# Kernel optimization log

Hardware: AMD Instinct MI355X
Metric: run time of the kernel (lower is better)

Reference implementation:

```python
import jax, jax.numpy as jnp
import numpy as np

B, Q, K, H = 4, 256, 256, 512
NEG = -1e9


def setup_inputs() -> dict:
    key = jax.random.key(0)
    ks = jax.random.split(key, 7)
    scale = 1.0 / np.sqrt(H)
    return {
        "query": jax.random.normal(ks[0], (B, Q, H), jnp.float32),
        "key": jax.random.normal(ks[1], (B, K, H), jnp.float32),
        "value": jax.random.normal(ks[2], (B, K, H), jnp.float32),
        "valid_lens": jax.random.randint(ks[3], (B,), 0, K, jnp.int32),
        "Wq": jax.random.normal(ks[4], (H, H), jnp.float32) * scale,
        "Wk": jax.random.normal(ks[5], (H, H), jnp.float32) * scale,
        "wv": jax.random.normal(ks[6], (H,), jnp.float32) * scale,
    }


def reference(query, key, value, valid_lens, Wq, Wk, wv):
    # projections (nn.Linear without bias)
    q = query @ Wq              # [B,Q,H]
    k = key @ Wk                # [B,K,H]
    # broadcast add + tanh: [B,Q,K,H]
    features = jnp.tanh(q[:, :, None, :] + k[:, None, :, :])
    # score projection w_v: [B,Q,K]
    scores = jnp.einsum("bqkh,h->bqk", features, wv)
    # sequence mask: positions >= valid_len masked out
    mask = jnp.arange(K)[None, :] >= valid_lens[:, None]   # [B,K]
    scores = jnp.where(mask[:, None, :], NEG, scores)
    attn = jax.nn.softmax(scores, axis=-1)                 # [B,Q,K]
    context = jnp.einsum("bqk,bkh->bqh", attn, value)      # [B,Q,H]
    return context
```

## Files before the change

kernel.cpp:

```cpp
#include <hip/hip_runtime.h>
#include <hip/hip_bf16.h>

#define B_ 4
#define Q_ 256
#define K_ 256
#define H_ 512
#define NEG (-1e9f)
#define PRESCALE 2.885390081777927f

typedef _Float16 half8 __attribute__((ext_vector_type(8)));
typedef float    f32x4 __attribute__((ext_vector_type(4)));

__global__ __launch_bounds__(256) void proj_kernel(
    const float* __restrict__ Xq, const float* __restrict__ Xk,
    const float* __restrict__ Wq, const float* __restrict__ Wk,
    float* __restrict__ Eq, float* __restrict__ EkT,
    const int* __restrict__ vlen)
{
    const int bx   = blockIdx.x;
    const int z    = bx >> 4;
    const int row0 = (bx & 15) * 64;
    const int bb   = row0 >> 8;
    const int k0   = row0 & 255;
    if (z && k0 >= vlen[bb]) return;

    const float* X = z ? Xk : Xq;
    const float* W = z ? Wk : Wq;

    __shared__ _Float16 Xl[4 * 520];
    __shared__ _Float16 Wl[4 * 520];

    const int col0 = blockIdx.y * 64;
    const int t    = threadIdx.x;
    const int lane = t & 63;
    const int w    = t >> 6;
    const int m    = lane & 15;
    const int kgl  = lane >> 4;

    const int xr  = t >> 2;
    const int xkg = t & 3;
    const int wc  = t & 63;
    const int wkg = t >> 6;

    f32x4 acc[4] = {};

    float4 xv0 = *(const float4*)&X[(size_t)(row0 + xr) * H_ + xkg * 8];
    float4 xv1 = *(const float4*)&X[(size_t)(row0 + xr) * H_ + xkg * 8 + 4];
    float wv8[8];
    #pragma unroll
    for (int i = 0; i < 8; ++i)
        wv8[i] = W[(size_t)(wkg * 8 + i) * H_ + col0 + wc];

    for (int it = 0; it < 16; ++it) {
        {
            half8 hx;
            hx[0] = (_Float16)xv0.x; hx[1] = (_Float16)xv0.y;
            hx[2] = (_Float16)xv0.z; hx[3] = (_Float16)xv0.w;
            hx[4] = (_Float16)xv1.x; hx[5] = (_Float16)xv1.y;
            hx[6] = (_Float16)xv1.z; hx[7] = (_Float16)xv1.w;
            *(half8*)&Xl[xkg * 520 + xr * 8] = hx;
            half8 hw;
            #pragma unroll
            for (int i = 0; i < 8; ++i) hw[i] = (_Float16)wv8[i];
            *(half8*)&Wl[wkg * 520 + wc * 8] = hw;
        }
        __syncthreads();
        if (it < 15) {
            const int kk = (it + 1) * 32;
            xv0 = *(const float4*)&X[(size_t)(row0 + xr) * H_ + kk + xkg * 8];
            xv1 = *(const float4*)&X[(size_t)(row0 + xr) * H_ + kk + xkg * 8 + 4];
            #pragma unroll
            for (int i = 0; i < 8; ++i)
                wv8[i] = W[(size_t)(kk + wkg * 8 + i) * H_ + col0 + wc];
        }
        const _Float16* Asrc = z ? Wl : Xl;
        const _Float16* Bsrc = z ? Xl : Wl;
        const half8 af = *(const half8*)&Asrc[kgl * 520 + (16 * w + m) * 8];
        #pragma unroll
        for (int nt = 0; nt < 4; ++nt) {
            const half8 bf = *(const half8*)&Bsrc[kgl * 520 + (nt * 16 + m) * 8];
            acc[nt] = __builtin_amdgcn_mfma_f32_16x16x32_f16(af, bf, acc[nt], 0, 0, 0);
        }
        __syncthreads();
    }

    if (!z) {
        #pragma unroll
        for (int nt = 0; nt < 4; ++nt) {
            const int gcol = col0 + nt * 16 + m;
            #pragma unroll
            for (int r = 0; r < 4; ++r) {
                const int grow = row0 + 16 * w + kgl * 4 + r;
                Eq[(size_t)grow * H_ + gcol] =
                    __builtin_amdgcn_exp2f(acc[nt][r] * PRESCALE);
            }
        }
    } else {
        #pragma unroll
        for (int nt = 0; nt < 4; ++nt) {
            const int gk = k0 + nt * 16 + m;
            #pragma unroll
            for (int r = 0; r < 4; ++r) {
                const int gh = col0 + 16 * w + kgl * 4 + r;
                EkT[((size_t)bb * H_ + gh) * K_ + gk] =
                    __builtin_amdgcn_exp2f(acc[nt][r] * PRESCALE);
            }
        }
    }
}

__global__ __launch_bounds__(512) void fused_attn(
    const float* __restrict__ Eq, const float* __restrict__ EkT,
    const float* __restrict__ value, const int* __restrict__ vlen,
    const float* __restrict__ wv, float* __restrict__ out)
{
    const int qt = blockIdx.x;
    const int b  = blockIdx.y;
    const int q0 = qt * 2;
    const int t    = threadIdx.x;
    const int wave = t >> 6;
    const int lane = t & 63;

    __shared__ float eqh[H_][2];
    __shared__ float wm[H_];
    __shared__ float sc[2][K_];
    __shared__ float ctxp[4][2][H_];

    const int valid = vlen[b];

    if (t < 256) {
        const int qi = t >> 7, p4 = (t & 127) * 4;
        const float4 v = *(const float4*)&Eq[((size_t)b * Q_ + q0 + qi) * H_ + p4];
        eqh[p4 + 0][qi] = v.x; eqh[p4 + 1][qi] = v.y;
        eqh[p4 + 2][qi] = v.z; eqh[p4 + 3][qi] = v.w;
    } else if (t < 384) {
        const int i = (t - 256) * 4;
        const float4 w = *(const float4*)&wv[i];
        *(float4*)&wm[i] = make_float4(-2.f * w.x, -2.f * w.y, -2.f * w.z, -2.f * w.w);
    }
    __syncthreads();

    const int band = wave * 32;
    const int ho   = lane >> 3;
    const int kg   = lane & 7;
    const int kq   = band + kg * 4;

    if (band < valid) {
        const float* ekp = EkT + ((size_t)b * H_ + ho) * K_ + kq;
        float a0[4] = {}, a1[4] = {};
        float4 pe[4], ne[4];
        #pragma unroll
        for (int p = 0; p < 4; ++p)
            pe[p] = *(const float4*)(ekp + (size_t)p * 8 * K_);

        for (int g = 0; g < 16; ++g) {
            if (g < 15) {
                #pragma unroll
                for (int p = 0; p < 4; ++p)
                    ne[p] = *(const float4*)(ekp + (size_t)((g + 1) * 4 + p) * 8 * K_);
            }
            #pragma unroll
            for (int p = 0; p < 4; ++p) {
                const int h = ho + 8 * (g * 4 + p);
                const float2 eq = *(const float2*)&eqh[h][0];
                const float  w  = wm[h];
                const float ek4[4] = {pe[p].x, pe[p].y, pe[p].z, pe[p].w};
                #pragma unroll
                for (int j = 0; j < 4; ++j) {
                    const float g0 = __builtin_fmaf(eq.x, ek4[j], 1.0f);
                    a0[j] = __builtin_fmaf(w, __builtin_amdgcn_rcpf(g0), a0[j]);
                    const float g1 = __builtin_fmaf(eq.y, ek4[j], 1.0f);
                    a1[j] = __builtin_fmaf(w, __builtin_amdgcn_rcpf(g1), a1[j]);
                }
            }
            if (g < 15) {
                #pragma unroll
                for (int p = 0; p < 4; ++p) pe[p] = ne[p];
            }
        }
        #pragma unroll
        for (int d = 8; d < 64; d <<= 1) {
            #pragma unroll
            for (int j = 0; j < 4; ++j) {
                a0[j] += __shfl_xor(a0[j], d);
                a1[j] += __shfl_xor(a1[j], d);
            }
        }
        if (ho == 0) {
            *(float4*)&sc[0][kq] = make_float4(a0[0], a0[1], a0[2], a0[3]);
            *(float4*)&sc[1][kq] = make_float4(a1[0], a1[1], a1[2], a1[3]);
        }
    }
    __syncthreads();

    if (wave < 2) {
        const int q = wave;
        if (valid == 0) {
            #pragma unroll
            for (int j = 0; j < 4; ++j) sc[q][lane + 64 * j] = 1.0f / K_;
        } else {
            float sv[4], mx = -3e38f;
            #pragma unroll
            for (int j = 0; j < 4; ++j) {
                const int kk = lane + 64 * j;
                const float s = (kk < valid) ? sc[q][kk] : NEG;
                sv[j] = s;
                mx = fmaxf(mx, s);
            }
            #pragma unroll
            for (int d = 32; d; d >>= 1) mx = fmaxf(mx, __shfl_xor(mx, d));
            float ev[4], sum = 0.f;
            #pragma unroll
            for (int j = 0; j < 4; ++j) { ev[j] = __expf(sv[j] - mx); sum += ev[j]; }
            #pragma unroll
            for (int d = 32; d; d >>= 1) sum += __shfl_xor(sum, d);
            const float inv = 1.0f / sum;
            #pragma unroll
            for (int j = 0; j < 4; ++j) sc[q][lane + 64 * j] = ev[j] * inv;
        }
    }
    __syncthreads();

    const int klim = (valid == 0) ? K_ : valid;
    const int kb   = wave * 32;
    const int kend = min(32, klim - kb);
    const int h0   = lane * 8;

    float c0[8] = {}, c1[8] = {};
    for (int kc = 0; kc < kend; ++kc) {
        const int kk = kb + kc;
        const float4* vp = (const float4*)&value[((size_t)b * K_ + kk) * H_ + h0];
        const float4 v0 = vp[0], v1 = vp[1];
        const float vr[8] = {v0.x, v0.y, v0.z, v0.w, v1.x, v1.y, v1.z, v1.w};
        const float a0 = sc[0][kk], a1 = sc[1][kk];
        #pragma unroll
        for (int j = 0; j < 8; ++j) {
            c0[j] = __builtin_fmaf(a0, vr[j], c0[j]);
            c1[j] = __builtin_fmaf(a1, vr[j], c1[j]);
        }
    }

    #define PARK(s)                                                         \
        do {                                                                \
            float* d0 = &ctxp[s][0][h0];                                    \
            float* d1 = &ctxp[s][1][h0];                                    \
            ((float4*)d0)[0] = make_float4(c0[0], c0[1], c0[2], c0[3]);     \
            ((float4*)d0)[1] = make_float4(c0[4], c0[5], c0[6], c0[7]);     \
            ((float4*)d1)[0] = make_float4(c1[0], c1[1], c1[2], c1[3]);     \
            ((float4*)d1)[1] = make_float4(c1[4], c1[5], c1[6], c1[7]);     \
        } while (0)
    #define FOLD(s)                                                         \
        do {                                                                \
            const float* d0 = &ctxp[s][0][h0];                              \
            const float* d1 = &ctxp[s][1][h0];                              \
            _Pragma("unroll")                                               \
            for (int j = 0; j < 8; ++j) { c0[j] += d0[j]; c1[j] += d1[j]; } \
        } while (0)

    if (wave >= 4) PARK(wave - 4);
    __syncthreads();
    if (wave < 4) FOLD(wave);
    __syncthreads();
    if (wave == 2 || wave == 3) PARK(wave - 2);
    __syncthreads();
    if (wave < 2) FOLD(wave);
    __syncthreads();
    if (wave == 1) PARK(1);
    __syncthreads();
    if (wave == 0) {
        FOLD(1);
        float* o0 = &out[((size_t)b * Q_ + q0 + 0) * H_ + h0];
        float* o1 = &out[((size_t)b * Q_ + q0 + 1) * H_ + h0];
        ((float4*)o0)[0] = make_float4(c0[0], c0[1], c0[2], c0[3]);
        ((float4*)o0)[1] = make_float4(c0[4], c0[5], c0[6], c0[7]);
        ((float4*)o1)[0] = make_float4(c1[0], c1[1], c1[2], c1[3]);
        ((float4*)o1)[1] = make_float4(c1[4], c1[5], c1[6], c1[7]);
    }
    #undef PARK
    #undef FOLD
}

extern "C" void kernel_launch(void* const* d_in, const int* in_sizes, int n_in,
                              void* d_out, int out_size, void* d_ws, size_t ws_size,
                              hipStream_t stream)
{
    const float* query = (const float*)d_in[0];
    const float* key   = (const float*)d_in[1];
    const float* value = (const float*)d_in[2];
    const int*   vlen  = (const int*)  d_in[3];
    const float* Wq    = (const float*)d_in[4];
    const float* Wk    = (const float*)d_in[5];
    const float* wv    = (const float*)d_in[6];
    float*       outp  = (float*)d_out;

    float* EqBuf  = (float*)d_ws;
    float* EkTBuf = EqBuf + (size_t)B_ * Q_ * H_;

    dim3 g1(32, 8);
    proj_kernel<<<g1, 256, 0, stream>>>(query, key, Wq, Wk, EqBuf, EkTBuf, vlen);

    dim3 g2(Q_ / 2, B_);
    fused_attn<<<g2, 512, 0, stream>>>(EqBuf, EkTBuf, value, vlen, wv, outp);
}
```

Measured before the change: 40.18 us.

## Double-buffer projection GEMM with 512 threads, deepen EkT prefetch, relayout LDS

The projection kernel now runs 512 threads with a 2x4 wave tiling, K-step 64, and double-buffered LDS, which removes the trailing barrier per iteration and halves loop trips. In the attention kernel, the Eq and weight vectors are relaid out in LDS so each thread reads contiguous float4s per group instead of scattered float2/float loads. The EkT prefetch is also deepened to two groups ahead. The cost is more registers and larger LDS, which could lower occupancy.

```diff
diff --git a/kernel.cpp b/kernel.cpp
--- a/kernel.cpp
+++ b/kernel.cpp
@@ -11,7 +11,7 @@
 typedef _Float16 half8 __attribute__((ext_vector_type(8)));
 typedef float    f32x4 __attribute__((ext_vector_type(4)));
 
-__global__ __launch_bounds__(256) void proj_kernel(
+__global__ __launch_bounds__(512) void proj_kernel(
     const float* __restrict__ Xq, const float* __restrict__ Xk,
     const float* __restrict__ Wq, const float* __restrict__ Wk,
     float* __restrict__ Eq, float* __restrict__ EkT,
@@ -27,84 +27,88 @@
     const float* X = z ? Xk : Xq;
     const float* W = z ? Wk : Wq;
 
-    __shared__ _Float16 Xl[4 * 520];
-    __shared__ _Float16 Wl[4 * 520];
+    __shared__ _Float16 Xl[2][8 * 520];
+    __shared__ _Float16 Wl[2][8 * 520];
 
     const int col0 = blockIdx.y * 64;
     const int t    = threadIdx.x;
     const int lane = t & 63;
-    const int w    = t >> 6;
+    const int wave = t >> 6;
+    const int mw   = wave >> 1;
+    const int nw   = wave & 1;
     const int m    = lane & 15;
     const int kgl  = lane >> 4;
 
-    const int xr  = t >> 2;
-    const int xkg = t & 3;
-    const int wc  = t & 63;
-    const int wkg = t >> 6;
-
-    f32x4 acc[4] = {};
-
-    float4 xv0 = *(const float4*)&X[(size_t)(row0 + xr) * H_ + xkg * 8];
-    float4 xv1 = *(const float4*)&X[(size_t)(row0 + xr) * H_ + xkg * 8 + 4];
+    const int xr = t >> 3;
+    const int xg = t & 7;
+    const int wc = t & 63;
+    const int wg = t >> 6;
+
+    f32x4 acc[2] = {};
+
+    float4 xv0 = *(const float4*)&X[(size_t)(row0 + xr) * H_ + xg * 8];
+    float4 xv1 = *(const float4*)&X[(size_t)(row0 + xr) * H_ + xg * 8 + 4];
     float wv8[8];
     #pragma unroll
     for (int i = 0; i < 8; ++i)
-        wv8[i] = W[(size_t)(wkg * 8 + i) * H_ + col0 + wc];
-
-    for (int it = 0; it < 16; ++it) {
+        wv8[i] = W[(size_t)(wg * 8 + i) * H_ + col0 + wc];
+
+    for (int it = 0; it < 8; ++it) {
+        const int buf = it & 1;
         {
             half8 hx;
             hx[0] = (_Float16)xv0.x; hx[1] = (_Float16)xv0.y;
             hx[2] = (_Float16)xv0.z; hx[3] = (_Float16)xv0.w;
             hx[4] = (_Float16)xv1.x; hx[5] = (_Float16)xv1.y;
             hx[6] = (_Float16)xv1.z; hx[7] = (_Float16)xv1.w;
-            *(half8*)&Xl[xkg * 520 + xr * 8] = hx;
+            *(half8*)&Xl[buf][xg * 520 + xr * 8] = hx;
             half8 hw;
             #pragma unroll
             for (int i = 0; i < 8; ++i) hw[i] = (_Float16)wv8[i];
-            *(half8*)&Wl[wkg * 520 + wc * 8] = hw;
+            *(half8*)&Wl[buf][wg * 520 + wc * 8] = hw;
         }
         __syncthreads();
-        if (it < 15) {
-            const int kk = (it + 1) * 32;
-            xv0 = *(const float4*)&X[(size_t)(row0 + xr) * H_ + kk + xkg * 8];
-            xv1 = *(const float4*)&X[(size_t)(row0 + xr) * H_ + kk + xkg * 8 + 4];
+        if (it < 7) {
+            const int kk = (it + 1) * 64;
+            xv0 = *(const float4*)&X[(size_t)(row0 + xr) * H_ + kk + xg * 8];
+            xv1 = *(const float4*)&X[(size_t)(row0 + xr) * H_ + kk + xg * 8 + 4];
             #pragma unroll
             for (int i = 0; i < 8; ++i)
-                wv8[i] = W[(size_t)(kk + wkg * 8 + i) * H_ + col0 + wc];
-        }
-        const _Float16* Asrc = z ? Wl : Xl;
-        const _Float16* Bsrc = z ? Xl : Wl;
-        const half8 af = *(const half8*)&Asrc[kgl * 520 + (16 * w + m) * 8];
-        #pragma unroll
-        for (int nt = 0; nt < 4; ++nt) {
-            const half8 bf = *(const half8*)&Bsrc[kgl * 520 + (nt * 16 + m) * 8];
-            acc[nt] = __builtin_amdgcn_mfma_f32_16x16x32_f16(af, bf, acc[nt], 0, 0, 0);
-        }
-        __syncthreads();
-    }
-
+                wv8[i] = W[(size_t)(kk + wg * 8 + i) * H_ + col0 + wc];
+        }
+        const _Float16* Asrc = z ? &Wl[buf][0] : &Xl[buf][0];
+        const _Float16* Bsrc = z ? &Xl[buf][0] : &Wl[buf][0];
+        #pragma unroll
+        for (int ks = 0; ks < 2; ++ks) {
+            const int slab = (ks * 4 + kgl) * 520;
+            const half8 af = *(const half8*)&Asrc[slab + (16 * mw + m) * 8];
+            #pragma unroll
+            for (int nt = 0; nt < 2; ++nt) {
+                const half8 bf =
+                    *(const half8*)&Bsrc[slab + (nw * 32 + nt * 16 + m) * 8];
+                acc[nt] = __builtin_amdgcn_mfma_f32_16x16x32_f16(af, bf, acc[nt], 0, 0, 0);
+            }
+        }
+    }
+
+    const int rloc = 16 * mw + kgl * 4;
     if (!z) {
         #pragma unroll
-        for (int nt = 0; nt < 4; ++nt) {
-            const int gcol = col0 + nt * 16 + m;
-            #pragma unroll
-            for (int r = 0; r < 4; ++r) {
-                const int grow = row0 + 16 * w + kgl * 4 + r;
-                Eq[(size_t)grow * H_ + gcol] =
+        for (int nt = 0; nt < 2; ++nt) {
+            const int gcol = col0 + nw * 32 + nt * 16 + m;
+            #pragma unroll
+            for (int r = 0; r < 4; ++r)
+                Eq[(size_t)(row0 + rloc + r) * H_ + gcol] =
                     __builtin_amdgcn_exp2f(acc[nt][r] * PRESCALE);
-            }
         }
     } else {
         #pragma unroll
-        for (int nt = 0; nt < 4; ++nt) {
-            const int gk = k0 + nt * 16 + m;
-            #pragma unroll
-            for (int r = 0; r < 4; ++r) {
-                const int gh = col0 + 16 * w + kgl * 4 + r;
-                EkT[((size_t)bb * H_ + gh) * K_ + gk] =
+        for (int nt = 0; nt < 2; ++nt) {
+            const int gk = k0 + nw * 32 + nt * 16 + m;
+            #pragma unroll
+            for (int r = 0; r < 4; ++r)
+                EkT[((size_t)bb * H_ + col0 + rloc + r) * K_ + gk] =
                     __builtin_amdgcn_exp2f(acc[nt][r] * PRESCALE);
-            }
         }
     }
 }
@@ -121,8 +125,8 @@
     const int wave = t >> 6;
     const int lane = t & 63;
 
-    __shared__ float eqh[H_][2];
-    __shared__ float wm[H_];
+    __shared__ float eqh2[8 * 132];
+    __shared__ float wm2[8 * 68];
     __shared__ float sc[2][K_];
     __shared__ float ctxp[4][2][H_];
 
@@ -131,12 +135,21 @@
     if (t < 256) {
         const int qi = t >> 7, p4 = (t & 127) * 4;
         const float4 v = *(const float4*)&Eq[((size_t)b * Q_ + q0 + qi) * H_ + p4];
-        eqh[p4 + 0][qi] = v.x; eqh[p4 + 1][qi] = v.y;
-        eqh[p4 + 2][qi] = v.z; eqh[p4 + 3][qi] = v.w;
+        const float vv[4] = {v.x, v.y, v.z, v.w};
+        #pragma unroll
+        for (int j = 0; j < 4; ++j) {
+            const int h = p4 + j;
+            eqh2[(h & 7) * 132 + (h >> 3) * 2 + qi] = vv[j];
+        }
     } else if (t < 384) {
         const int i = (t - 256) * 4;
         const float4 w = *(const float4*)&wv[i];
-        *(float4*)&wm[i] = make_float4(-2.f * w.x, -2.f * w.y, -2.f * w.z, -2.f * w.w);
+        const float ww[4] = {w.x, w.y, w.z, w.w};
+        #pragma unroll
+        for (int j = 0; j < 4; ++j) {
+            const int h = i + j;
+            wm2[(h & 7) * 68 + (h >> 3)] = -2.f * ww[j];
+        }
     }
     __syncthreads();
 
@@ -148,35 +161,39 @@
     if (band < valid) {
         const float* ekp = EkT + ((size_t)b * H_ + ho) * K_ + kq;
         float a0[4] = {}, a1[4] = {};
-        float4 pe[4], ne[4];
+        float4 pe[4], n1[4], n2[4];
         #pragma unroll
         for (int p = 0; p < 4; ++p)
             pe[p] = *(const float4*)(ekp + (size_t)p * 8 * K_);
+        #pragma unroll
+        for (int p = 0; p < 4; ++p)
+            n1[p] = *(const float4*)(ekp + (size_t)(4 + p) * 8 * K_);
 
         for (int g = 0; g < 16; ++g) {
-            if (g < 15) {
+            if (g < 14) {
                 #pragma unroll
                 for (int p = 0; p < 4; ++p)
-                    ne[p] = *(const float4*)(ekp + (size_t)((g + 1) * 4 + p) * 8 * K_);
-            }
+                    n2[p] = *(const float4*)(ekp + (size_t)((g + 2) * 4 + p) * 8 * K_);
+            }
+            const float4 eqA = *(const float4*)&eqh2[ho * 132 + g * 8];
+            const float4 eqB = *(const float4*)&eqh2[ho * 132 + g * 8 + 4];
+            const float4 wv4 = *(const float4*)&wm2[ho * 68 + g * 4];
+            const float eq0[4] = {eqA.x, eqA.z, eqB.x, eqB.z};
+            const float eq1[4] = {eqA.y, eqA.w, eqB.y, eqB.w};
+            const float wmp[4] = {wv4.x, wv4.y, wv4.z, wv4.w};
             #pragma unroll
             for (int p = 0; p < 4; ++p) {
-                const int h = ho + 8 * (g * 4 + p);
-                const float2 eq = *(const float2*)&eqh[h][0];
-                const float  w  = wm[h];
                 const float ek4[4] = {pe[p].x, pe[p].y, pe[p].z, pe[p].w};
                 #pragma unroll
                 for (int j = 0; j < 4; ++j) {
-                    const float g0 = __builtin_fmaf(eq.x, ek4[j], 1.0f);
-                    a0[j] = __builtin_fmaf(w, __builtin_amdgcn_rcpf(g0), a0[j]);
-                    const float g1 = __builtin_fmaf(eq.y, ek4[j], 1.0f);
-                    a1[j] = __builtin_fmaf(w, __builtin_amdgcn_rcpf(g1), a1[j]);
+                    const float g0 = __builtin_fmaf(eq0[p], ek4[j], 1.0f);
+                    a0[j] = __builtin_fmaf(wmp[p], __builtin_amdgcn_rcpf(g0), a0[j]);
+                    const float g1 = __builtin_fmaf(eq1[p], ek4[j], 1.0f);
+                    a1[j] = __builtin_fmaf(wmp[p], __builtin_amdgcn_rcpf(g1), a1[j]);
                 }
             }
-            if (g < 15) {
-                #pragma unroll
-                for (int p = 0; p < 4; ++p) pe[p] = ne[p];
-            }
+            #pragma unroll
+            for (int p = 0; p < 4; ++p) { pe[p] = n1[p]; n1[p] = n2[p]; }
         }
         #pragma unroll
         for (int d = 8; d < 64; d <<= 1) {
@@ -297,7 +314,7 @@
     float* EkTBuf = EqBuf + (size_t)B_ * Q_ * H_;
 
     dim3 g1(32, 8);
-    proj_kernel<<<g1, 256, 0, stream>>>(query, key, Wq, Wk, EqBuf, EkTBuf, vlen);
+    proj_kernel<<<g1, 512, 0, stream>>>(query, key, Wq, Wk, EqBuf, EkTBuf, vlen);
 
     dim3 g2(Q_ / 2, B_);
     fused_attn<<<g2, 512, 0, stream>>>(EqBuf, EkTBuf, value, vlen, wv, outp);
```

Measured after the change: 37.11 us. 7.6% less time.
